# Kernel optimization log

Hardware: AMD Instinct MI355X
Metric: run time of the kernel (lower is better)

## Reference

```python
import jax, jax.numpy as jnp
import numpy as np

B, T, N_EMBD, HEAD = 8, 2048, 1024, 64
NEG_INF = -1e30  # stand-in for float('-inf'), safe under fp16/bf16 after where


def setup_inputs() -> dict:
    key = jax.random.key(0)
    k0, k1, k2, k3 = jax.random.split(key, 4)
    idx = jax.random.normal(k0, (B, T, N_EMBD), dtype=jnp.float32)
    # nn.Linear weights have shape (out_features, in_features)
    Wk = jax.random.normal(k1, (HEAD, N_EMBD), dtype=jnp.float32) * 0.02
    Wq = jax.random.normal(k2, (HEAD, N_EMBD), dtype=jnp.float32) * 0.02
    Wv = jax.random.normal(k3, (HEAD, N_EMBD), dtype=jnp.float32) * 0.02
    return {"idx": idx, "Wk": Wk, "Wq": Wq, "Wv": Wv}


def reference(idx, Wk, Wq, Wv):
    # idx: [B,T,C]; W*: [H,C] (torch Linear layout, y = x @ W.T)
    Tn = idx.shape[1]
    k = jnp.einsum('btc,hc->bth', idx, Wk)
    q = jnp.einsum('btc,hc->bth', idx, Wq)
    v = jnp.einsum('btc,hc->bth', idx, Wv)
    # NOTE: original has NO 1/sqrt(head_size) scaling
    wei = jnp.einsum('bth,bsh->bts', q, k)  # [B,T,T]
    causal = jnp.tril(jnp.ones((Tn, Tn), dtype=bool))  # keep where tril != 0
    wei = jnp.where(causal[None, :, :], wei, NEG_INF)
    # NOTE: original softmaxes over dim=1 (query axis), not the last axis
    wei = jax.nn.softmax(wei, axis=1)
    out = jnp.einsum('bts,bsh->bth', wei, v)  # [B,T,H]
    return out
```

## Files before the change

kernel.cpp:

```cpp
#include <hip/hip_runtime.h>


typedef __attribute__((ext_vector_type(8))) short bf16x8;
typedef __attribute__((ext_vector_type(4))) float f32x4;
typedef unsigned short u16;

#define MFMA(a, b, c) __builtin_amdgcn_mfma_f32_16x16x32_bf16((a), (b), (c), 0, 0, 0)

__device__ __forceinline__ u16 f2bf(float x) {
    unsigned u = __float_as_uint(x);
    u += 0x7fff + ((u >> 16) & 1);
    return (u16)(u >> 16);
}
__device__ __forceinline__ float bf2f(u16 h) {
    return __uint_as_float(((unsigned)h) << 16);
}

__device__ __forceinline__ void split8(const f32x4 x0, const f32x4 x1,
                                       bf16x8* hv, bf16x8* lv)
{
    const float f[8] = {x0[0], x0[1], x0[2], x0[3], x1[0], x1[1], x1[2], x1[3]};
    union { unsigned u[4]; bf16x8 v; } H, L;
    #pragma unroll
    for (int j = 0; j < 4; ++j) {
        const unsigned u0 = __float_as_uint(f[2 * j]);
        const unsigned u1 = __float_as_uint(f[2 * j + 1]);
        H.u[j] = __builtin_amdgcn_perm(u1, u0, 0x07060302);
        const float l0 = f[2 * j]     - __uint_as_float(u0 & 0xffff0000u);
        const float l1 = f[2 * j + 1] - __uint_as_float(u1 & 0xffff0000u);
        L.u[j] = __builtin_amdgcn_perm(__float_as_uint(l1), __float_as_uint(l0),
                                       0x07060302);
    }
    *hv = H.v;
    *lv = L.v;
}

typedef const __attribute__((address_space(1))) void* gas_p;
typedef __attribute__((address_space(3))) void* las_p;

#define WH_OFF  0u
#define WL_OFF  (WH_OFF + 192u*1024u*2u)
#define FQH_OFF (WL_OFF + 192u*1024u*2u)
#define FQL_OFF (FQH_OFF + 2u*1024u*1024u)
#define FKH_OFF (FQL_OFF + 2u*1024u*1024u)
#define FKL_OFF (FKH_OFF + 2u*1024u*1024u)
#define VF_OFF  (FKL_OFF + 2u*1024u*1024u)
#define DD_OFF  (VF_OFF + 2u*1024u*1024u)
#define PF_OFF  (DD_OFF + 8u*2048u*4u)

__global__ __launch_bounds__(128) void wsplit_kernel(
    const float* __restrict__ Wk, const float* __restrict__ Wq,
    const float* __restrict__ Wv, u16* __restrict__ FWH)
{
    const int n = blockIdx.x;
    const int nblk = n >> 4, lr = n & 15;
    const float* src = (n < 64) ? (Wq + (long)n * 1024)
                     : (n < 128) ? (Wk + (long)(n - 64) * 1024)
                                 : (Wv + (long)(n - 128) * 1024);
    const int f = threadIdx.x;
    const int kc = f >> 2, q = f & 3;
    const float4 f0 = *(const float4*)&src[kc * 32 + q * 8];
    const float4 f1 = *(const float4*)&src[kc * 32 + q * 8 + 4];
    const float vs[8] = {f0.x, f0.y, f0.z, f0.w, f1.x, f1.y, f1.z, f1.w};
    bf16x8 hv;
    #pragma unroll
    for (int j = 0; j < 8; ++j) hv[j] = (short)f2bf(vs[j]);
    const long o = ((long)(nblk * 32 + kc) * 64 + q * 16 + lr) * 8;
    *(bf16x8*)&FWH[o] = hv;
}

__global__ __launch_bounds__(512, 2) void qkv_kernel(
    const float* __restrict__ idx, const u16* __restrict__ FWH,
    u16* __restrict__ FQH, u16* __restrict__ FQL,
    u16* __restrict__ FKH, u16* __restrict__ FKL, u16* __restrict__ VF)
{
    __shared__ __align__(16) char smem[3][40960];
    const int tid = threadIdx.x;
    const int w = tid >> 6, lr = tid & 15, quad = (tid >> 4) & 3;
    const int lane = tid & 63;
    const int r0 = blockIdx.x * 64;
    const int b = r0 >> 11, t0 = r0 & 2047;
    const int m0 = (w & 1) * 32;
    const int nbb = (w >> 1) * 3;

    const float* asrc[2];
    int adst[2];
    #pragma unroll
    for (int j = 0; j < 2; ++j) {
        const int s = w * 2 + j;
        const int row = s * 4 + (lane >> 4);
        const int lc = (lane & 15) ^ (row & 7);
        asrc[j] = idx + (long)(r0 + row) * 1024 + lc * 4;
        adst[j] = s * 1024;
    }
    const u16* fsrc[3];
    int fdst[3];
    #pragma unroll
    for (int j = 0; j < 3; ++j) {
        const int seg = w * 3 + j;
        const int nblk = seg >> 1, kcl = seg & 1;
        fsrc[j] = FWH + (long)nblk * 16384 + kcl * 512 + lane * 8;
        fdst[j] = 16384 + seg * 1024;
    }

#define ISSUE(PH)                                                             \
    {                                                                         \
        const int nb_ = (PH) % 3;                                             \
        _Pragma("unroll")                                                     \
        for (int j = 0; j < 2; ++j)                                           \
            __builtin_amdgcn_global_load_lds((gas_p)(asrc[j] + (PH) * 64),    \
                (las_p)(smem[nb_] + adst[j]), 16, 0, 0);                      \
        _Pragma("unroll")                                                     \
        for (int j = 0; j < 3; ++j)                                           \
            __builtin_amdgcn_global_load_lds((gas_p)(fsrc[j] + (long)(PH) * 1024), \
                (las_p)(smem[nb_] + fdst[j]), 16, 0, 0);                      \
    }

#define COMPUTE(PH)                                                           \
    {                                                                         \
        const int nb_ = (PH) % 3;                                             \
        const float* A_ = (const float*)smem[nb_];                            \
        const u16* F_ = (const u16*)(smem[nb_] + 16384);                      \
        _Pragma("unroll")                                                     \
        for (int kc = 0; kc < 2; ++kc) {                                      \
            bf16x8 AH[2], AL[2];                                              \
            _Pragma("unroll")                                                 \
            for (int mi = 0; mi < 2; ++mi) {                                  \
                const int R = m0 + mi * 16 + lr;                              \
                const int c0 = (kc * 8 + quad * 2) ^ (lr & 7);                \
                const f32x4 x0 = *(const f32x4*)&A_[R * 64 + c0 * 4];         \
                const f32x4 x1 = *(const f32x4*)&A_[R * 64 + (c0 ^ 1) * 4];   \
                split8(x0, x1, &AH[mi], &AL[mi]);                             \
            }                                                                 \
            _Pragma("unroll")                                                 \
            for (int nf = 0; nf < 3; ++nf) {                                  \
                const int sb = (((nbb + nf) * 2 + kc)) * 512 + lane * 8;      \
                const bf16x8 bh = *(const bf16x8*)&F_[sb];                    \
                _Pragma("unroll")                                             \
                for (int mi = 0; mi < 2; ++mi) {                              \
                    f32x4 c = acc[mi][nf];                                    \
                    c = MFMA(AH[mi], bh, c);                                  \
                    c = MFMA(AL[mi], bh, c);                                  \
                    acc[mi][nf] = c;                                          \
                }                                                             \
            }                                                                 \
        }                                                                     \
    }

#define WAITV(N)                                                              \
    asm volatile("s_waitcnt vmcnt(" #N ")" ::: "memory");                     \
    __builtin_amdgcn_sched_barrier(0);                                        \
    __builtin_amdgcn_s_barrier();

    f32x4 acc[2][3] = {};

    ISSUE(0); ISSUE(1);
    WAITV(5)

    for (int ph = 0; ph < 14; ++ph) {
        ISSUE(ph + 2);
        __builtin_amdgcn_sched_barrier(0);
        COMPUTE(ph);
        WAITV(5)
    }
    COMPUTE(14);
    WAITV(0)
    COMPUTE(15);

#undef WAITV
#undef COMPUTE
#undef ISSUE

    #pragma unroll
    for (int mi = 0; mi < 2; ++mi) {
        const int tb = t0 + m0 + mi * 16 + quad * 4;
        const int tblk = (t0 + m0 + mi * 16) >> 4;
        #pragma unroll
        for (int nf = 0; nf < 3; ++nf) {
            const int n = (nbb + nf) * 16 + lr;
            const f32x4 a = acc[mi][nf];
            if (n < 128) {
                u16* Hd = (n < 64) ? FQH : FKH;
                u16* Ld = (n < 64) ? FQL : FKL;
                const int h = n & 63;
                const int kc = h >> 5;
                const int lsub = 16 * ((h & 31) >> 3);
                const long base = ((long)(b * 128 + tblk) * 2 + kc) * 512 + (h & 7);
                #pragma unroll
                for (int r = 0; r < 4; ++r) {
                    const float v = a[r];
                    const u16 hi = f2bf(v);
                    const u16 lo = f2bf(v - bf2f(hi));
                    const long o = base + (long)(quad * 4 + r + lsub) * 8;
                    Hd[o] = hi; Ld[o] = lo;
                }
            } else {
                const int h = n - 128;
                const int hblk = h >> 4;
                #pragma unroll
                for (int r = 0; r < 4; ++r) {
                    const int t = tb + r;
                    const long o = ((long)(b * 4 + hblk) * 64 + (t >> 5)) * 512
                                 + (long)(16 * ((t & 31) >> 3) + (h & 15)) * 8 + (t & 7);
                    VF[o] = f2bf(a[r]);
                }
            }
        }
    }
}

__global__ __launch_bounds__(256, 4) void stats_kernel(
    const u16* __restrict__ FQH, const u16* __restrict__ FQL,
    const u16* __restrict__ FKH, const u16* __restrict__ FKL,
    u16* __restrict__ PF, float* __restrict__ D)
{
    __shared__ float red[4][64];
    const int tid = threadIdx.x;
    const int w = tid >> 6, lr = tid & 15, quad = (tid >> 4) & 3;
    const int lane = tid & 63;
    const int b = blockIdx.y;
    int x = blockIdx.x, i = 0;
    for (;;) { const int nc = (35 - i) >> 2; if (x < nc) break; x -= nc; ++i; }
    const int s0 = i * 64;
    const int jt0 = i + 4 * x, jt1 = min(jt0 + 4, 32);

    bf16x8 BH[4][2], BL[4][2];
    #pragma unroll
    for (int nf = 0; nf < 4; ++nf) {
        const long kb = ((long)(b * 128 + i * 4 + nf) * 2) * 512 + lane * 8;
        BH[nf][0] = *(const bf16x8*)&FKH[kb];
        BH[nf][1] = *(const bf16x8*)&FKH[kb + 512];
        BL[nf][0] = *(const bf16x8*)&FKL[kb];
        BL[nf][1] = *(const bf16x8*)&FKL[kb + 512];
    }

    float dsum[4] = {0.f, 0.f, 0.f, 0.f};
    for (int jt = jt0; jt < jt1; ++jt) {
        const long qb = ((long)(b * 128 + jt * 4 + w) * 2) * 512 + lane * 8;
        const bf16x8 ah0 = *(const bf16x8*)&FQH[qb];
        const bf16x8 ah1 = *(const bf16x8*)&FQH[qb + 512];
        const bf16x8 al0 = *(const bf16x8*)&FQL[qb];
        const bf16x8 al1 = *(const bf16x8*)&FQL[qb + 512];
        const bool diag = (jt == i);
        #pragma unroll
        for (int nf = 0; nf < 4; ++nf) {
            f32x4 cc = {};
            cc = MFMA(ah0, BH[nf][0], cc);
            cc = MFMA(al0, BH[nf][0], cc);
            cc = MFMA(ah0, BL[nf][0], cc);
            cc = MFMA(ah1, BH[nf][1], cc);
            cc = MFMA(al1, BH[nf][1], cc);
            cc = MFMA(ah1, BL[nf][1], cc);

            const long pbase = ((long)(b * 128 + jt * 4 + w) * 64 + i * 2 + (nf >> 1)) * 512
                             + (long)(((nf & 1) * 2 + (lr >> 3)) * 16) * 8 + (lr & 7);
            const int sl = nf * 16 + lr;
            #pragma unroll
            for (int r = 0; r < 4; ++r) {
                float ev = __expf(cc[r]);
                if (diag && (w * 16 + quad * 4 + r < sl)) ev = 0.f;
                dsum[nf] += ev;
                PF[pbase + (long)(quad * 4 + r) * 8] = f2bf(ev);
            }
        }
    }

    #pragma unroll
    for (int nf = 0; nf < 4; ++nf) {
        dsum[nf] += __shfl_xor(dsum[nf], 16);
        dsum[nf] += __shfl_xor(dsum[nf], 32);
    }
    if (quad == 0) {
        #pragma unroll
        for (int nf = 0; nf < 4; ++nf) red[w][nf * 16 + lr] = dsum[nf];
    }
    __syncthreads();
    if (tid < 64)
        atomicAdd(&D[b * 2048 + s0 + tid],
                  red[0][tid] + red[1][tid] + red[2][tid] + red[3][tid]);
}

__global__ __launch_bounds__(256) void vscale_kernel(
    u16* __restrict__ VF, const float* __restrict__ D)
{
    const int g = blockIdx.x * 256 + threadIdx.x;
    const long e = (long)g * 8;
    const int lane = (int)((e >> 3) & 63);
    const int kc   = (int)((e >> 9) & 63);
    const int b    = (int)(e >> 17);
    const int s = kc * 32 + (lane >> 4) * 8;
    const float4 d0 = *(const float4*)&D[b * 2048 + s];
    const float4 d1 = *(const float4*)&D[b * 2048 + s + 4];
    const float dv[8] = {d0.x, d0.y, d0.z, d0.w, d1.x, d1.y, d1.z, d1.w};
    bf16x8 vv = *(bf16x8*)&VF[e];
    bf16x8 ov;
    #pragma unroll
    for (int j = 0; j < 8; ++j)
        ov[j] = (short)f2bf(bf2f((u16)vv[j]) / dv[j]);
    *(bf16x8*)&VF[e] = ov;
}

__global__ __launch_bounds__(256, 4) void out_kernel(
    const u16* __restrict__ PF, const u16* __restrict__ VF,
    float* __restrict__ out)
{
    const int tid = threadIdx.x;
    const int w = tid >> 6, lr = tid & 15, quad = (tid >> 4) & 3;
    const int lane = tid & 63;
    const int b = blockIdx.y;
    int x = blockIdx.x, i = 0;
    for (;;) { const int nc = (i + 8) >> 3; if (x < nc) break; x -= nc; ++i; }
    const int t0 = i * 64;
    const int js0 = 8 * x, js1 = min(8 * x + 8, i + 1);
    const int tblk = i * 4 + w;

    f32x4 oacc[4] = {};
    for (int js = js0; js < js1; ++js) {
        const long pb = ((long)(b * 128 + tblk) * 64 + 2 * js) * 512 + lane * 8;
        const bf16x8 a0 = *(const bf16x8*)&PF[pb];
        const bf16x8 a1 = *(const bf16x8*)&PF[pb + 512];
        #pragma unroll
        for (int nf = 0; nf < 4; ++nf) {
            const long vb = ((long)(b * 4 + nf) * 64 + 2 * js) * 512 + lane * 8;
            const bf16x8 v0 = *(const bf16x8*)&VF[vb];
            const bf16x8 v1 = *(const bf16x8*)&VF[vb + 512];
            oacc[nf] = MFMA(a0, v0, oacc[nf]);
            oacc[nf] = MFMA(a1, v1, oacc[nf]);
        }
    }

    const bool single = (i < 8);
    #pragma unroll
    for (int nf = 0; nf < 4; ++nf) {
        const int h = nf * 16 + lr;
        #pragma unroll
        for (int r = 0; r < 4; ++r) {
            const int t = t0 + w * 16 + quad * 4 + r;
            const long o = (long)(b * 2048 + t) * 64 + h;
            if (single) out[o] = oacc[nf][r];
            else        atomicAdd(&out[o], oacc[nf][r]);
        }
    }
}

extern "C" void kernel_launch(void* const* d_in, const int* in_sizes, int n_in,
                              void* d_out, int out_size, void* d_ws, size_t ws_size,
                              hipStream_t stream)
{
    const float* idx = (const float*)d_in[0];
    const float* Wk  = (const float*)d_in[1];
    const float* Wq  = (const float*)d_in[2];
    const float* Wv  = (const float*)d_in[3];
    char* ws = (char*)d_ws;
    float* out = (float*)d_out;

    u16* FWH = (u16*)(ws + WH_OFF);
    u16* FQH = (u16*)(ws + FQH_OFF); u16* FQL = (u16*)(ws + FQL_OFF);
    u16* FKH = (u16*)(ws + FKH_OFF); u16* FKL = (u16*)(ws + FKL_OFF);
    u16* VF  = (u16*)(ws + VF_OFF);
    float* Dp = (float*)(ws + DD_OFF);
    u16* PF  = (u16*)(ws + PF_OFF);

    hipMemsetAsync(out, 0, (size_t)8 * 2048 * 64 * sizeof(float), stream);
    hipMemsetAsync(Dp, 0, (size_t)8 * 2048 * sizeof(float), stream);

    wsplit_kernel<<<192, 128, 0, stream>>>(Wk, Wq, Wv, FWH);
    qkv_kernel<<<256, 512, 0, stream>>>(idx, FWH, FQH, FQL, FKH, FKL, VF);
    stats_kernel<<<dim3(144, 8), 256, 0, stream>>>(FQH, FQL, FKH, FKL, PF, Dp);
    vscale_kernel<<<512, 256, 0, stream>>>(VF, Dp);
    out_kernel<<<dim3(80, 8), 256, 0, stream>>>(PF, VF, out);
}
```

Before: 153.8 us.

## Stage exp'd scores in swizzled LDS to emit coalesced 16-byte P stores

The stats kernel now swaps the MFMA operand order so each lane holds consecutive key positions, packs four bf16 probabilities per lane into an XOR-swizzled shared-memory tile, then reads back full 16-byte rows and writes them to the fragment-layout P buffer as vector stores. This replaces the earlier scattered 2-byte global stores. The column-sum reduction is reorganized to match the transposed accumulator layout. The cost is two block barriers per query tile and extra LDS traffic.

```diff
diff --git a/kernel.cpp b/kernel.cpp
--- a/kernel.cpp
+++ b/kernel.cpp
@@ -215,6 +215,7 @@
     u16* __restrict__ PF, float* __restrict__ D)
 {
     __shared__ float red[4][64];
+    __shared__ __align__(16) u16 p_l[64 * 64];
     const int tid = threadIdx.x;
     const int w = tid >> 6, lr = tid & 15, quad = (tid >> 4) & 3;
     const int lane = tid & 63;
@@ -224,55 +225,82 @@
     const int s0 = i * 64;
     const int jt0 = i + 4 * x, jt1 = min(jt0 + 4, 32);
 
-    bf16x8 BH[4][2], BL[4][2];
-    #pragma unroll
-    for (int nf = 0; nf < 4; ++nf) {
-        const long kb = ((long)(b * 128 + i * 4 + nf) * 2) * 512 + lane * 8;
-        BH[nf][0] = *(const bf16x8*)&FKH[kb];
-        BH[nf][1] = *(const bf16x8*)&FKH[kb + 512];
-        BL[nf][0] = *(const bf16x8*)&FKL[kb];
-        BL[nf][1] = *(const bf16x8*)&FKL[kb + 512];
-    }
-
-    float dsum[4] = {0.f, 0.f, 0.f, 0.f};
+    bf16x8 KH[4][2], KL[4][2];
+    #pragma unroll
+    for (int sf = 0; sf < 4; ++sf) {
+        const long kb = ((long)(b * 128 + i * 4 + sf) * 2) * 512 + lane * 8;
+        KH[sf][0] = *(const bf16x8*)&FKH[kb];
+        KH[sf][1] = *(const bf16x8*)&FKH[kb + 512];
+        KL[sf][0] = *(const bf16x8*)&FKL[kb];
+        KL[sf][1] = *(const bf16x8*)&FKL[kb + 512];
+    }
+
+    float dsum[4][4] = {};
     for (int jt = jt0; jt < jt1; ++jt) {
         const long qb = ((long)(b * 128 + jt * 4 + w) * 2) * 512 + lane * 8;
-        const bf16x8 ah0 = *(const bf16x8*)&FQH[qb];
-        const bf16x8 ah1 = *(const bf16x8*)&FQH[qb + 512];
-        const bf16x8 al0 = *(const bf16x8*)&FQL[qb];
-        const bf16x8 al1 = *(const bf16x8*)&FQL[qb + 512];
+        const bf16x8 qh0 = *(const bf16x8*)&FQH[qb];
+        const bf16x8 qh1 = *(const bf16x8*)&FQH[qb + 512];
+        const bf16x8 ql0 = *(const bf16x8*)&FQL[qb];
+        const bf16x8 ql1 = *(const bf16x8*)&FQL[qb + 512];
         const bool diag = (jt == i);
-        #pragma unroll
-        for (int nf = 0; nf < 4; ++nf) {
+        const int t_sub = w * 16 + lr;
+        #pragma unroll
+        for (int sf = 0; sf < 4; ++sf) {
             f32x4 cc = {};
-            cc = MFMA(ah0, BH[nf][0], cc);
-            cc = MFMA(al0, BH[nf][0], cc);
-            cc = MFMA(ah0, BL[nf][0], cc);
-            cc = MFMA(ah1, BH[nf][1], cc);
-            cc = MFMA(al1, BH[nf][1], cc);
-            cc = MFMA(ah1, BL[nf][1], cc);
-
-            const long pbase = ((long)(b * 128 + jt * 4 + w) * 64 + i * 2 + (nf >> 1)) * 512
-                             + (long)(((nf & 1) * 2 + (lr >> 3)) * 16) * 8 + (lr & 7);
-            const int sl = nf * 16 + lr;
+            cc = MFMA(KH[sf][0], qh0, cc);
+            cc = MFMA(KH[sf][0], ql0, cc);
+            cc = MFMA(KL[sf][0], qh0, cc);
+            cc = MFMA(KH[sf][1], qh1, cc);
+            cc = MFMA(KH[sf][1], ql1, cc);
+            cc = MFMA(KL[sf][1], qh1, cc);
+
+            u16 hq[4];
             #pragma unroll
             for (int r = 0; r < 4; ++r) {
                 float ev = __expf(cc[r]);
-                if (diag && (w * 16 + quad * 4 + r < sl)) ev = 0.f;
-                dsum[nf] += ev;
-                PF[pbase + (long)(quad * 4 + r) * 8] = f2bf(ev);
+                if (diag && (t_sub < sf * 16 + quad * 4 + r)) ev = 0.f;
+                dsum[sf][r] += ev;
+                hq[r] = f2bf(ev);
             }
-        }
-    }
-
-    #pragma unroll
-    for (int nf = 0; nf < 4; ++nf) {
-        dsum[nf] += __shfl_xor(dsum[nf], 16);
-        dsum[nf] += __shfl_xor(dsum[nf], 32);
-    }
-    if (quad == 0) {
-        #pragma unroll
-        for (int nf = 0; nf < 4; ++nf) red[w][nf * 16 + lr] = dsum[nf];
+            const int s_sub = sf * 16 + quad * 4;
+            const int ch = (s_sub >> 3) ^ (t_sub & 7);
+            const int aoff = t_sub * 64 + ch * 8 + (s_sub & 7);
+            uint2 pk;
+            pk.x = (unsigned)hq[0] | ((unsigned)hq[1] << 16);
+            pk.y = (unsigned)hq[2] | ((unsigned)hq[3] << 16);
+            *(uint2*)&p_l[aoff] = pk;
+        }
+        __syncthreads();
+        #pragma unroll
+        for (int kcp = 0; kcp < 2; ++kcp) {
+            const int row = w * 16 + (lane & 15);
+            const int sc = kcp * 32 + (lane >> 4) * 8;
+            const int ch = (sc >> 3) ^ (row & 7);
+            const bf16x8 v = *(const bf16x8*)&p_l[row * 64 + ch * 8];
+            const long o = ((long)(b * 128 + jt * 4 + w) * 64 + i * 2 + kcp) * 512
+                         + lane * 8;
+            *(bf16x8*)&PF[o] = v;
+        }
+        __syncthreads();
+    }
+
+    #pragma unroll
+    for (int sf = 0; sf < 4; ++sf)
+        #pragma unroll
+        for (int r = 0; r < 4; ++r) {
+            float v = dsum[sf][r];
+            v += __shfl_xor(v, 1);
+            v += __shfl_xor(v, 2);
+            v += __shfl_xor(v, 4);
+            v += __shfl_xor(v, 8);
+            dsum[sf][r] = v;
+        }
+    if (lr == 0) {
+        #pragma unroll
+        for (int sf = 0; sf < 4; ++sf)
+            #pragma unroll
+            for (int r = 0; r < 4; ++r)
+                red[w][sf * 16 + quad * 4 + r] = dsum[sf][r];
     }
     __syncthreads();
     if (tid < 64)
```

Measured after the change: 149.8 us. -2.6%, faster.
